# Optimization experiments

Hardware: AMD Instinct MI355X
Metric: run time of the kernel (lower is better)

The kernel has to match this reference:

```python
import jax, jax.numpy as jnp
import numpy as np

N, E, L, H, D_HID, D_IN, D_NEI, S_NEI, N_CLS = 30000, 480000, 2, 4, 128, 128, 64, 10, 2
HD = D_HID // H  # 32 per-head dim


def _mha(x, in_w, in_b, out_w, out_b, n_heads=4):
    # x: [N, S, D]; in_w: [D, 3D]; out_w: [D, D]
    n, s, d = x.shape
    hd = d // n_heads
    qkv = x @ in_w + in_b  # [N, S, 3D]
    q, k, v = jnp.split(qkv, 3, axis=-1)
    rs = lambda t: t.reshape(n, s, n_heads, hd).transpose(0, 2, 1, 3)  # [N,H,S,hd]
    q, k, v = rs(q), rs(k), rs(v)
    attn = jax.nn.softmax(jnp.einsum('nhqd,nhkd->nhqk', q, k) / np.sqrt(hd).astype(np.float32), axis=-1)
    o = jnp.einsum('nhqk,nhkd->nhqd', attn, v).transpose(0, 2, 1, 3).reshape(n, s, d)
    return o @ out_w + out_b


def _layer_norm(x, g, b, eps=1e-5):
    m = jnp.mean(x, axis=-1, keepdims=True)
    v = jnp.var(x, axis=-1, keepdims=True)
    return (x - m) * jax.lax.rsqrt(v + eps) * g + b


def _transformer_conv(src, dst, h, wq_i, bq_i, wk_i, bk_i, wv_i, bv_i):
    # per-head graph transformer conv: q from dst, k/v from src, edge softmax over dst
    q = (h @ wq_i + bq_i).reshape(N, H, HD)
    k = (h @ wk_i + bk_i).reshape(N, H, HD)
    v = (h @ wv_i + bv_i).reshape(N, H, HD)
    score = jnp.sum(q[dst] * k[src], axis=-1) / np.sqrt(HD).astype(np.float32)  # [E, H]
    smax = jax.ops.segment_max(score, dst, num_segments=N)  # [N, H]
    ex = jnp.exp(score - smax[dst])  # [E, H]
    denom = jax.ops.segment_sum(ex, dst, num_segments=N)  # [N, H]
    num = jax.ops.segment_sum(ex[:, :, None] * v[src], dst, num_segments=N)  # [N, H, HD]
    out = num / jnp.maximum(denom, 1e-9)[:, :, None]
    return out.reshape(N, D_HID)


def setup_inputs() -> dict:
    key = jax.random.key(0)
    ks = jax.random.split(key, 24)
    d = {}
    d['x'] = jax.random.normal(ks[0], (N, D_IN), jnp.float32)
    d['nei_features'] = jax.random.normal(ks[1], (N, S_NEI, D_NEI), jnp.float32)
    d['edge_index'] = jax.random.randint(ks[2], (L, 2, E), 0, N, jnp.int32)
    sc = 0.05
    d['w_in'] = jax.random.normal(ks[3], (D_IN, D_HID), jnp.float32) * sc
    d['b_in'] = jax.random.normal(ks[4], (D_HID,), jnp.float32) * sc
    d['mha_in_w'] = jax.random.normal(ks[5], (D_NEI, 3 * D_NEI), jnp.float32) * sc
    d['mha_in_b'] = jax.random.normal(ks[6], (3 * D_NEI,), jnp.float32) * sc
    d['mha_out_w'] = jax.random.normal(ks[7], (D_NEI, D_NEI), jnp.float32) * sc
    d['mha_out_b'] = jax.random.normal(ks[8], (D_NEI,), jnp.float32) * sc
    d['w_nei'] = jax.random.normal(ks[9], (D_NEI, D_HID), jnp.float32) * sc
    d['b_nei'] = jax.random.normal(ks[10], (D_HID,), jnp.float32) * sc
    d['wq'] = jax.random.normal(ks[11], (L, D_HID, D_HID), jnp.float32) * sc
    d['bq'] = jax.random.normal(ks[12], (L, D_HID), jnp.float32) * sc
    d['wk'] = jax.random.normal(ks[13], (L, D_HID, D_HID), jnp.float32) * sc
    d['bk'] = jax.random.normal(ks[14], (L, D_HID), jnp.float32) * sc
    d['wv'] = jax.random.normal(ks[15], (L, D_HID, D_HID), jnp.float32) * sc
    d['bv'] = jax.random.normal(ks[16], (L, D_HID), jnp.float32) * sc
    d['ln_g'] = jnp.ones((L, D_HID), jnp.float32)
    d['ln_b'] = jnp.zeros((L, D_HID), jnp.float32)
    d['w_out'] = jax.random.normal(ks[17], (D_HID, N_CLS), jnp.float32) * sc
    d['b_out'] = jnp.zeros((N_CLS,), jnp.float32)
    return d


def reference(x, nei_features, edge_index, w_in, b_in, mha_in_w, mha_in_b,
              mha_out_w, mha_out_b, w_nei, b_nei, wq, bq, wk, bk, wv, bv,
              ln_g, ln_b, w_out, b_out):
    h = x @ w_in + b_in  # input_proj
    # neighbor-feature self-attention branch (nn.MultiheadAttention, eval mode)
    nei = _mha(nei_features, mha_in_w, mha_in_b, mha_out_w, mha_out_b).mean(axis=1)
    h = h + (nei @ w_nei + b_nei)
    for i in range(L):
        src, dst = edge_index[i, 0], edge_index[i, 1]
        h = _transformer_conv(src, dst, h, wq[i], bq[i], wk[i], bk[i], wv[i], bv[i])
        h = jax.nn.relu(h)
        h = _layer_norm(h, ln_g[i], ln_b[i])
        # dropout is identity in eval mode
    return h @ w_out + b_out
```

## Files before the change

### kernel.cpp

```cpp
#include <hip/hip_runtime.h>
#include <hip/hip_bf16.h>

#define NN 30000
#define EE 480000

typedef __attribute__((ext_vector_type(8))) short short8;
typedef __attribute__((ext_vector_type(4))) short short4v;
typedef __attribute__((ext_vector_type(4))) float floatx4;
typedef unsigned short u16;

__device__ __forceinline__ u16 f2bf(float f) {
  union { float f; unsigned u; } v; v.f = f;
  unsigned u = v.u;
  u += 0x7FFFu + ((u >> 16) & 1u);
  return (u16)(u >> 16);
}
__device__ __forceinline__ float bf2f(u16 u) {
  union { unsigned u; float f; } v; v.u = ((unsigned)u) << 16;
  return v.f;
}
__device__ __forceinline__ float bflo(unsigned u) {
  union { unsigned x; float f; } v; v.x = u << 16; return v.f;
}
__device__ __forceinline__ float bfhi(unsigned u) {
  union { unsigned x; float f; } v; v.x = u & 0xFFFF0000u; return v.f;
}
__device__ __forceinline__ unsigned packbf(float a, float b) {
  return (unsigned)f2bf(a) | ((unsigned)f2bf(b) << 16);
}
__device__ __forceinline__ short8 pack8(float4 A, float4 B) {
  union { unsigned u[4]; short8 s; } r;
  r.u[0] = packbf(A.x, A.y);
  r.u[1] = packbf(A.z, A.w);
  r.u[2] = packbf(B.x, B.y);
  r.u[3] = packbf(B.z, B.w);
  return r.s;
}

template <int CTRL>
__device__ __forceinline__ float dppadd(float v) {
  int s = __builtin_amdgcn_update_dpp(0, __builtin_bit_cast(int, v), CTRL, 0xF, 0xF, true);
  return v + __builtin_bit_cast(float, s);
}
__device__ __forceinline__ float rowsum16(float v) {
  v = dppadd<0x121>(v); v = dppadd<0x122>(v); v = dppadd<0x124>(v); v = dppadd<0x128>(v);
  return v;
}
__device__ __forceinline__ float rowsum8(float v) {
  v = dppadd<0xB1>(v); v = dppadd<0x4E>(v); v = dppadd<0x141>(v);
  return v;
}

#define MFMA32 __builtin_amdgcn_mfma_f32_16x16x32_bf16

#if __has_builtin(__builtin_amdgcn_mfma_f32_16x16x16bf16_1k)
__device__ __forceinline__ floatx4 MFMA16(short4v a, short4v b, floatx4 c) {
  return __builtin_amdgcn_mfma_f32_16x16x16bf16_1k(a, b, c, 0, 0, 0);
}
#else
__device__ __forceinline__ floatx4 MFMA16(short4v a, short4v b, floatx4 c) {
  asm volatile("v_mfma_f32_16x16x16_bf16 %0, %1, %2, %0"
               : "+v"(c) : "v"(a), "v"(b));
  return c;
}
#endif

__global__ __launch_bounds__(128) void k_fuse(
    const float* __restrict__ out_w, const float* __restrict__ out_b,
    const float* __restrict__ w_nei, const float* __restrict__ b_nei,
    const float* __restrict__ b_in,
    float* __restrict__ fusedW, float* __restrict__ fusedB) {
  int i = blockIdx.x, j = threadIdx.x;
  if (i < 64) {
    float a = 0.f;
    for (int kk = 0; kk < 64; ++kk) a = fmaf(out_w[i * 64 + kk], w_nei[kk * 128 + j], a);
    fusedW[i * 128 + j] = a;
  } else {
    float a = b_in[j] + b_nei[j];
    for (int kk = 0; kk < 64; ++kk) a = fmaf(out_b[kk], w_nei[kk * 128 + j], a);
    fusedB[j] = a;
  }
}

__global__ __launch_bounds__(128) void k_prepB(
    const float* __restrict__ in_w, const float* __restrict__ fusedW,
    const float* __restrict__ fusedB, const float* __restrict__ in_b,
    float* __restrict__ G, float* __restrict__ fusedB2) {
  int bx = blockIdx.x, c = threadIdx.x;
  if (bx < 256) {
    int h = bx >> 6, d = bx & 63;
    float a = 0.f;
    for (int dd = 0; dd < 16; ++dd)
      a = fmaf(in_w[d * 192 + 128 + h * 16 + dd], fusedW[(h * 16 + dd) * 128 + c], a);
    G[bx * 128 + c] = a;
  } else {
    float a = fusedB[c];
    for (int d = 0; d < 64; ++d) a = fmaf(in_b[128 + d], fusedW[d * 128 + c], a);
    fusedB2[c] = a;
  }
}

__global__ __launch_bounds__(384) void k_prepP2(
    const float* __restrict__ w_in, const float* __restrict__ G,
    u16* __restrict__ wtP2) {
  int c = blockIdx.x, k = threadIdx.x;
  float v = (k < 128) ? w_in[(size_t)k * 128 + c] : G[(size_t)(k - 128) * 128 + c];
  wtP2[(size_t)c * 384 + k] = f2bf(v);
}

__global__ __launch_bounds__(128) void k_prepA(
    const float* __restrict__ wq, const float* __restrict__ wk,
    const float* __restrict__ wv, const float* __restrict__ in_w,
    u16* __restrict__ wt3, u16* __restrict__ wtQK) {
  int bx = blockIdx.x, t = threadIdx.x;
  if (bx < 768) {
    int l = bx / 384, rem = bx % 384, o = rem >> 7, c = rem & 127;
    const float* w = (o == 0 ? wq : (o == 1 ? wk : wv)) + (size_t)l * 16384;
    wt3[(size_t)bx * 128 + t] = f2bf(w[(size_t)t * 128 + c]);
  } else {
    int c = (bx - 768) * 2 + (t >> 6), kk = t & 63;
    float s = (c < 64) ? 0.25f : 1.f;
    wtQK[(size_t)c * 64 + kk] = f2bf(s * in_w[(size_t)kk * 192 + c]);
  }
}

__global__ __launch_bounds__(640) void k_mha7(
    const float* __restrict__ xn,
    const u16* __restrict__ wtQK,
    const float* __restrict__ in_b,
    u16* __restrict__ Yb) {
  __shared__ unsigned qks[112 * 66];
  __shared__ u16 xsT[64 * 160];
  int t = threadIdx.x, w = t >> 6, l = t & 63;
  int lr = l & 15, lq = l >> 4;
  const floatx4 zf = {0.f, 0.f, 0.f, 0.f};
  size_t r0 = (size_t)blockIdx.x * 100;

  {
    int d = t / 10, nd = t - d * 10;
#pragma unroll
    for (int j = 10; j < 16; ++j) xsT[d * 160 + nd * 16 + j] = 0;
  }

  if (w < 7) {
    int row = w * 16 + lr;
    size_t arow = r0 + row;
    if (arow > 299999) arow = 299999;
    const float* xp = xn + arow * 64 + lq * 8;
    float4 f0 = *(const float4*)xp;
    float4 f1 = *(const float4*)(xp + 4);
    float4 f2 = *(const float4*)(xp + 32);
    float4 f3 = *(const float4*)(xp + 36);
    short8 a0 = pack8(f0, f1), a1 = pack8(f2, f3);
    if (row < 100) {
      int node = row / 10, j = row - node * 10;
      int base = node * 16 + j;
      union { short8 s; u16 u[8]; } ua0, ua1;
      ua0.s = a0; ua1.s = a1;
#pragma unroll
      for (int i = 0; i < 8; ++i) {
        xsT[(lq * 8 + i) * 160 + base] = ua0.u[i];
        xsT[(32 + lq * 8 + i) * 160 + base] = ua1.u[i];
      }
    }
    floatx4 acc[8];
#pragma unroll
    for (int ct = 0; ct < 8; ++ct) acc[ct] = zf;
#pragma unroll
    for (int ct = 0; ct < 8; ++ct) {
      const short8* bp = (const short8*)(wtQK + (size_t)(ct * 16 + lr) * 64);
      acc[ct] = MFMA32(a0, bp[lq], acc[ct], 0, 0, 0);
      acc[ct] = MFMA32(a1, bp[4 + lq], acc[ct], 0, 0, 0);
    }
#pragma unroll
    for (int ct = 0; ct < 4; ++ct) {
      float bq_ = in_b[ct * 16 + lr] * 0.25f;
      float bk_ = in_b[64 + ct * 16 + lr];
#pragma unroll
      for (int r = 0; r < 4; ++r)
        qks[(w * 16 + lq * 4 + r) * 66 + ct * 16 + lr] =
            packbf(acc[ct][r] + bq_, acc[ct + 4][r] + bk_);
    }
  }
  __syncthreads();

  int seqc = lr < 10 ? lr : 9;
  {
    float af0 = 0.f, af1 = 0.f, af2 = 0.f, af3 = 0.f;
#pragma unroll
    for (int h = 0; h < 4; ++h) {
      const unsigned* rp = &qks[(w * 10 + seqc) * 66 + h * 16 + lq * 4];
      uint2 u0 = *(const uint2*)rp;
      uint2 u1 = *(const uint2*)(rp + 2);
      union { unsigned u[2]; short4v s; } qv, kv;
      qv.u[0] = (u0.x & 0xFFFFu) | (u0.y << 16);
      qv.u[1] = (u1.x & 0xFFFFu) | (u1.y << 16);
      kv.u[0] = (u0.x >> 16) | (u0.y & 0xFFFF0000u);
      kv.u[1] = (u1.x >> 16) | (u1.y & 0xFFFF0000u);
      floatx4 s4 = MFMA16(kv.s, qv.s, zf);
      int j0 = lq * 4;
      float e0 = (j0 + 0 < 10) ? __expf(s4[0]) : 0.f;
      float e1 = (j0 + 1 < 10) ? __expf(s4[1]) : 0.f;
      float e2 = (j0 + 2 < 10) ? __expf(s4[2]) : 0.f;
      float e3 = (j0 + 3 < 10) ? __expf(s4[3]) : 0.f;
      float den = e0 + e1 + e2 + e3;
      den += __shfl_xor(den, 16, 64);
      den += __shfl_xor(den, 32, 64);
      float rden = 0.1f / den;
      float v0 = (lr < 10) ? e0 * rden : 0.f;
      float v1 = (lr < 10) ? e1 * rden : 0.f;
      float v2 = (lr < 10) ? e2 * rden : 0.f;
      float v3 = (lr < 10) ? e3 * rden : 0.f;
      v0 = rowsum16(v0);
      v1 = rowsum16(v1);
      v2 = rowsum16(v2);
      v3 = rowsum16(v3);
      if (lr == h) { af0 = v0; af1 = v1; af2 = v2; af3 = v3; }
    }
    union { unsigned u[2]; short4v s; } afv;
    afv.u[0] = packbf(af0, af1);
    afv.u[1] = packbf(af2, af3);
    size_t node = (size_t)blockIdx.x * 10 + w;
#pragma unroll
    for (int ct = 0; ct < 4; ++ct) {
      short4v bx = *(const short4v*)&xsT[(ct * 16 + lr) * 160 + w * 16 + lq * 4];
      floatx4 y4 = MFMA16(afv.s, bx, zf);
      if (lq == 0) {
        size_t yb = node * 256;
#pragma unroll
        for (int r = 0; r < 4; ++r)
          Yb[yb + r * 64 + ct * 16 + lr] = f2bf(y4[r]);
      }
    }
  }
}

__global__ __launch_bounds__(256) void k_proj5(
    const float* __restrict__ x, const u16* __restrict__ Yb,
    const u16* __restrict__ wtP2, const float* __restrict__ fusedB2,
    u16* __restrict__ hb) {
  int t = threadIdx.x, w = t >> 6, l = t & 63, lr = l & 15, lq = l >> 4;
  int row0 = blockIdx.x * 64 + w * 16;
  int arow = row0 + lr; if (arow >= NN) arow = NN - 1;
  const float* xp = x + (size_t)arow * 128;
  const short8* yp = (const short8*)(Yb + (size_t)arow * 256);
  short8 afr[12];
#pragma unroll
  for (int kb = 0; kb < 4; ++kb) {
    float4 fa = *(const float4*)(xp + kb * 32 + lq * 8);
    float4 fb = *(const float4*)(xp + kb * 32 + lq * 8 + 4);
    afr[kb] = pack8(fa, fb);
  }
#pragma unroll
  for (int m = 0; m < 8; ++m) afr[4 + m] = yp[m * 4 + lq];
  floatx4 acc[8];
#pragma unroll
  for (int ct = 0; ct < 8; ++ct) acc[ct] = (floatx4){0.f, 0.f, 0.f, 0.f};
#pragma unroll
  for (int ct = 0; ct < 8; ++ct) {
    const short8* bp = (const short8*)(wtP2 + (size_t)(ct * 16 + lr) * 384);
#pragma unroll
    for (int kb = 0; kb < 12; ++kb)
      acc[ct] = MFMA32(afr[kb], bp[kb * 4 + lq], acc[ct], 0, 0, 0);
  }
#pragma unroll
  for (int ct = 0; ct < 8; ++ct) {
    int col = ct * 16 + lr;
    float bias = fusedB2[col];
#pragma unroll
    for (int r = 0; r < 4; ++r) {
      int row = row0 + lq * 4 + r;
      if (row < NN) hb[(size_t)row * 128 + col] = f2bf(acc[ct][r] + bias);
    }
  }
}

__global__ __launch_bounds__(256) void k_qkv4(
    const u16* __restrict__ hb, const u16* __restrict__ wt3l,
    const float* __restrict__ bqL, const float* __restrict__ bkL,
    const float* __restrict__ bvL,
    unsigned* __restrict__ q2, unsigned* __restrict__ k2, unsigned* __restrict__ v2) {
  int t = threadIdx.x, w = t >> 6, l = t & 63, lr = l & 15, lq = l >> 4;
  int row0 = blockIdx.x * 64 + w * 16;
  int arow = row0 + lr; if (arow >= NN) arow = NN - 1;
  const short8* ap = (const short8*)(hb + (size_t)arow * 128);
  short8 a0 = ap[lq], a1 = ap[4 + lq], a2 = ap[8 + lq], a3 = ap[12 + lq];
  const short8* wt8 = (const short8*)wt3l;
  floatx4 acc[24];
#pragma unroll
  for (int ct = 0; ct < 24; ++ct) acc[ct] = (floatx4){0.f, 0.f, 0.f, 0.f};
#pragma unroll
  for (int ct = 0; ct < 24; ++ct) {
    const short8* bp = wt8 + (size_t)((ct >> 3) * 128 + (ct & 7) * 16 + lr) * 16;
    acc[ct] = MFMA32(a0, bp[lq], acc[ct], 0, 0, 0);
    acc[ct] = MFMA32(a1, bp[4 + lq], acc[ct], 0, 0, 0);
    acc[ct] = MFMA32(a2, bp[8 + lq], acc[ct], 0, 0, 0);
    acc[ct] = MFMA32(a3, bp[12 + lq], acc[ct], 0, 0, 0);
  }
#pragma unroll
  for (int o = 0; o < 3; ++o) {
    unsigned* op = o == 0 ? q2 : (o == 1 ? k2 : v2);
    const float* bp2 = o == 0 ? bqL : (o == 1 ? bkL : bvL);
#pragma unroll
    for (int cc = 0; cc < 4; ++cc) {
      int col = cc * 16 + lr;
      float blo = bp2[col], bhi = bp2[64 + col];
      floatx4 alo = acc[o * 8 + cc], ahi = acc[o * 8 + cc + 4];
#pragma unroll
      for (int r = 0; r < 4; ++r) {
        int row = row0 + lq * 4 + r;
        if (row < NN)
          op[(size_t)row * 64 + col] = packbf(alo[r] + blo, ahi[r] + bhi);
      }
    }
  }
}

__global__ __launch_bounds__(256) void k_fill(const int* __restrict__ ei,
                                              int* __restrict__ cnt,
                                              int* __restrict__ esrc) {
  int gthr = blockIdx.x * 256 + threadIdx.x;
  if (gthr < 2 * EE) {
    int l = gthr >= EE;
    int e = gthr - l * EE;
    int s = ei[(size_t)(2 * l) * EE + e];
    int d = ei[(size_t)(2 * l + 1) * EE + e];
    int c = atomicAdd(&cnt[l * NN + d], 1);
    if (c < 64) esrc[((size_t)l * NN + d) * 64 + c] = s;
  }
}

__global__ __launch_bounds__(256) void k_sagg7(
    const unsigned* __restrict__ q2, const unsigned* __restrict__ k2,
    const unsigned* __restrict__ v2, const int* __restrict__ esrc,
    const int* __restrict__ cnt, const float* __restrict__ g,
    const float* __restrict__ bb, u16* __restrict__ hb,
    const float* __restrict__ wo, const float* __restrict__ bo,
    float* __restrict__ outp) {
  const float SC = 0.17677669529663687f;
  int t = threadIdx.x, w = t >> 6, l = t & 63;
  int e = l >> 4, dd = l & 15;
  int n = blockIdx.x * 4 + w;
  int deg = cnt[n]; if (deg > 64) deg = 64;
  const int* sp = esrc + (size_t)n * 64;
  uint4 qp = *(const uint4*)(q2 + (size_t)n * 64 + dd * 4);
  float ql0 = bflo(qp.x), ql1 = bflo(qp.y), ql2 = bflo(qp.z), ql3 = bflo(qp.w);
  float qh0 = bfhi(qp.x), qh1 = bfhi(qp.y), qh2 = bfhi(qp.z), qh3 = bfhi(qp.w);
  float dA0 = 0.f, dA1 = 0.f, dB0 = 0.f, dB1 = 0.f;
  float alA0 = 0.f, alA1 = 0.f, alA2 = 0.f, alA3 = 0.f;
  float ahA0 = 0.f, ahA1 = 0.f, ahA2 = 0.f, ahA3 = 0.f;
  float alB0 = 0.f, alB1 = 0.f, alB2 = 0.f, alB3 = 0.f;
  float ahB0 = 0.f, ahB1 = 0.f, ahB2 = 0.f, ahB3 = 0.f;
  uint4 kA = {0, 0, 0, 0}, vA = {0, 0, 0, 0};
  uint4 kB = {0, 0, 0, 0}, vB = {0, 0, 0, 0};
  bool mA = false, mB = false;
  if (deg > 0) {
    int iA = e < deg ? e : deg - 1;           mA = e < deg;
    int iB = 4 + e < deg ? 4 + e : deg - 1;   mB = 4 + e < deg;
    int sA = sp[iA], sB = sp[iB];
    kA = *(const uint4*)(k2 + (size_t)sA * 64 + dd * 4);
    vA = *(const uint4*)(v2 + (size_t)sA * 64 + dd * 4);
    kB = *(const uint4*)(k2 + (size_t)sB * 64 + dd * 4);
    vB = *(const uint4*)(v2 + (size_t)sB * 64 + dd * 4);
  }
  for (int base = 0; base < deg; base += 8) {
    uint4 kAn = {0, 0, 0, 0}, vAn = {0, 0, 0, 0};
    uint4 kBn = {0, 0, 0, 0}, vBn = {0, 0, 0, 0};
    bool mAn = false, mBn = false;
    int nb = base + 8;
    if (nb < deg) {
      int iA = nb + e < deg ? nb + e : deg - 1;         mAn = nb + e < deg;
      int iB = nb + 4 + e < deg ? nb + 4 + e : deg - 1; mBn = nb + 4 + e < deg;
      int sA = sp[iA], sB = sp[iB];
      kAn = *(const uint4*)(k2 + (size_t)sA * 64 + dd * 4);
      vAn = *(const uint4*)(v2 + (size_t)sA * 64 + dd * 4);
      kBn = *(const uint4*)(k2 + (size_t)sB * 64 + dd * 4);
      vBn = *(const uint4*)(v2 + (size_t)sB * 64 + dd * 4);
    }
    float rA0 = ql0 * bflo(kA.x) + ql1 * bflo(kA.y) + ql2 * bflo(kA.z) + ql3 * bflo(kA.w);
    float rA1 = qh0 * bfhi(kA.x) + qh1 * bfhi(kA.y) + qh2 * bfhi(kA.z) + qh3 * bfhi(kA.w);
    float rB0 = ql0 * bflo(kB.x) + ql1 * bflo(kB.y) + ql2 * bflo(kB.z) + ql3 * bflo(kB.w);
    float rB1 = qh0 * bfhi(kB.x) + qh1 * bfhi(kB.y) + qh2 * bfhi(kB.z) + qh3 * bfhi(kB.w);
    rA0 = rowsum8(rA0); rA1 = rowsum8(rA1);
    rB0 = rowsum8(rB0); rB1 = rowsum8(rB1);
    float pA0 = mA ? __expf(rA0 * SC) : 0.f;
    float pA1 = mA ? __expf(rA1 * SC) : 0.f;
    float pB0 = mB ? __expf(rB0 * SC) : 0.f;
    float pB1 = mB ? __expf(rB1 * SC) : 0.f;
    dA0 += pA0; dA1 += pA1; dB0 += pB0; dB1 += pB1;
    alA0 = fmaf(pA0, bflo(vA.x), alA0); alA1 = fmaf(pA0, bflo(vA.y), alA1);
    alA2 = fmaf(pA0, bflo(vA.z), alA2); alA3 = fmaf(pA0, bflo(vA.w), alA3);
    ahA0 = fmaf(pA1, bfhi(vA.x), ahA0); ahA1 = fmaf(pA1, bfhi(vA.y), ahA1);
    ahA2 = fmaf(pA1, bfhi(vA.z), ahA2); ahA3 = fmaf(pA1, bfhi(vA.w), ahA3);
    alB0 = fmaf(pB0, bflo(vB.x), alB0); alB1 = fmaf(pB0, bflo(vB.y), alB1);
    alB2 = fmaf(pB0, bflo(vB.z), alB2); alB3 = fmaf(pB0, bflo(vB.w), alB3);
    ahB0 = fmaf(pB1, bfhi(vB.x), ahB0); ahB1 = fmaf(pB1, bfhi(vB.y), ahB1);
    ahB2 = fmaf(pB1, bfhi(vB.z), ahB2); ahB3 = fmaf(pB1, bfhi(vB.w), ahB3);
    kA = kAn; vA = vAn; mA = mAn;
    kB = kBn; vB = vBn; mB = mBn;
  }
  float d0 = dA0 + dB0, d1 = dA1 + dB1;
  float al0 = alA0 + alB0, al1 = alA1 + alB1, al2 = alA2 + alB2, al3 = alA3 + alB3;
  float ah0 = ahA0 + ahB0, ah1 = ahA1 + ahB1, ah2 = ahA2 + ahB2, ah3 = ahA3 + ahB3;
  d0 += __shfl_xor(d0, 16, 64); d0 += __shfl_xor(d0, 32, 64);
  d1 += __shfl_xor(d1, 16, 64); d1 += __shfl_xor(d1, 32, 64);
  al0 += __shfl_xor(al0, 16, 64); al0 += __shfl_xor(al0, 32, 64);
  al1 += __shfl_xor(al1, 16, 64); al1 += __shfl_xor(al1, 32, 64);
  al2 += __shfl_xor(al2, 16, 64); al2 += __shfl_xor(al2, 32, 64);
  al3 += __shfl_xor(al3, 16, 64); al3 += __shfl_xor(al3, 32, 64);
  ah0 += __shfl_xor(ah0, 16, 64); ah0 += __shfl_xor(ah0, 32, 64);
  ah1 += __shfl_xor(ah1, 16, 64); ah1 += __shfl_xor(ah1, 32, 64);
  ah2 += __shfl_xor(ah2, 16, 64); ah2 += __shfl_xor(ah2, 32, 64);
  ah3 += __shfl_xor(ah3, 16, 64); ah3 += __shfl_xor(ah3, 32, 64);
  float rd0 = 1.f / fmaxf(d0, 1e-9f), rd1 = 1.f / fmaxf(d1, 1e-9f);
  float ol0 = fmaxf(al0 * rd0, 0.f), ol1 = fmaxf(al1 * rd0, 0.f);
  float ol2 = fmaxf(al2 * rd0, 0.f), ol3 = fmaxf(al3 * rd0, 0.f);
  float oh0 = fmaxf(ah0 * rd1, 0.f), oh1 = fmaxf(ah1 * rd1, 0.f);
  float oh2 = fmaxf(ah2 * rd1, 0.f), oh3 = fmaxf(ah3 * rd1, 0.f);
  float s1 = ol0 + ol1 + ol2 + ol3 + oh0 + oh1 + oh2 + oh3;
  float s2 = ol0 * ol0 + ol1 * ol1 + ol2 * ol2 + ol3 * ol3 +
             oh0 * oh0 + oh1 * oh1 + oh2 * oh2 + oh3 * oh3;
  s1 = rowsum16(s1);
  s2 = rowsum16(s2);
  float mean = s1 * (1.f / 128.f);
  float var = s2 * (1.f / 128.f) - mean * mean;
  float rs = rsqrtf(var + 1e-5f);
  if (e == 0) {
    floatx4 gl = *(const floatx4*)(g + dd * 4);
    floatx4 bl = *(const floatx4*)(bb + dd * 4);
    floatx4 gh = *(const floatx4*)(g + 64 + dd * 4);
    floatx4 bh = *(const floatx4*)(bb + 64 + dd * 4);
    float hl0 = (ol0 - mean) * rs * gl[0] + bl[0];
    float hl1 = (ol1 - mean) * rs * gl[1] + bl[1];
    float hl2 = (ol2 - mean) * rs * gl[2] + bl[2];
    float hl3 = (ol3 - mean) * rs * gl[3] + bl[3];
    float hh0 = (oh0 - mean) * rs * gh[0] + bh[0];
    float hh1 = (oh1 - mean) * rs * gh[1] + bh[1];
    float hh2 = (oh2 - mean) * rs * gh[2] + bh[2];
    float hh3 = (oh3 - mean) * rs * gh[3] + bh[3];
    if (outp == nullptr) {
      uint2 w0, w1;
      w0.x = packbf(hl0, hl1); w0.y = packbf(hl2, hl3);
      w1.x = packbf(hh0, hh1); w1.y = packbf(hh2, hh3);
      *(uint2*)(hb + (size_t)n * 128 + dd * 4) = w0;
      *(uint2*)(hb + (size_t)n * 128 + 64 + dd * 4) = w1;
    } else {
      const float2* wo2 = (const float2*)wo;
      float2 wa0 = wo2[dd * 4], wa1 = wo2[dd * 4 + 1];
      float2 wa2 = wo2[dd * 4 + 2], wa3 = wo2[dd * 4 + 3];
      float2 wb0 = wo2[64 + dd * 4], wb1 = wo2[64 + dd * 4 + 1];
      float2 wb2 = wo2[64 + dd * 4 + 2], wb3 = wo2[64 + dd * 4 + 3];
      float p0 = hl0 * wa0.x + hl1 * wa1.x + hl2 * wa2.x + hl3 * wa3.x +
                 hh0 * wb0.x + hh1 * wb1.x + hh2 * wb2.x + hh3 * wb3.x;
      float p1 = hl0 * wa0.y + hl1 * wa1.y + hl2 * wa2.y + hl3 * wa3.y +
                 hh0 * wb0.y + hh1 * wb1.y + hh2 * wb2.y + hh3 * wb3.y;
      p0 = rowsum16(p0);
      p1 = rowsum16(p1);
      if (dd == 0) {
        outp[n * 2] = p0 + bo[0];
        outp[n * 2 + 1] = p1 + bo[1];
      }
    }
  }
}

extern "C" void kernel_launch(void* const* d_in, const int* in_sizes, int n_in,
                              void* d_out, int out_size, void* d_ws, size_t ws_size,
                              hipStream_t stream) {
  const float* x = (const float*)d_in[0];
  const float* neif = (const float*)d_in[1];
  const int* ei = (const int*)d_in[2];
  const float* w_in = (const float*)d_in[3];
  const float* b_in = (const float*)d_in[4];
  const float* mha_in_w = (const float*)d_in[5];
  const float* mha_in_b = (const float*)d_in[6];
  const float* mha_out_w = (const float*)d_in[7];
  const float* mha_out_b = (const float*)d_in[8];
  const float* w_nei = (const float*)d_in[9];
  const float* b_nei = (const float*)d_in[10];
  const float* wq = (const float*)d_in[11];
  const float* bq = (const float*)d_in[12];
  const float* wk = (const float*)d_in[13];
  const float* bk = (const float*)d_in[14];
  const float* wv = (const float*)d_in[15];
  const float* bv = (const float*)d_in[16];
  const float* ln_g = (const float*)d_in[17];
  const float* ln_b = (const float*)d_in[18];
  const float* w_out = (const float*)d_in[19];
  const float* b_out = (const float*)d_in[20];
  float* out = (float*)d_out;

  char* wsb = (char*)d_ws;
  size_t off = 0;
  unsigned* q2 = (unsigned*)(wsb + off); off += (size_t)NN * 64 * 4;
  unsigned* k2 = (unsigned*)(wsb + off); off += (size_t)NN * 64 * 4;
  unsigned* v2 = (unsigned*)(wsb + off); off += (size_t)NN * 64 * 4;
  int* esrc = (int*)(wsb + off);         off += (size_t)2 * NN * 64 * 4;
  u16* Yb = (u16*)(wsb + off);           off += (size_t)NN * 256 * 2;
  u16* hb = (u16*)(wsb + off);           off += (size_t)NN * 128 * 2;
  u16* wt3 = (u16*)(wsb + off);          off += (size_t)768 * 128 * 2;
  u16* wtP2 = (u16*)(wsb + off);         off += (size_t)128 * 384 * 2;
  u16* wtQK = (u16*)(wsb + off);         off += (size_t)128 * 64 * 2;
  float* G = (float*)(wsb + off);        off += (size_t)256 * 128 * 4;
  float* fusedW = (float*)(wsb + off);   off += 64 * 128 * 4;
  float* fusedB = (float*)(wsb + off);   off += 128 * 4;
  float* fusedB2 = (float*)(wsb + off);  off += 128 * 4;
  int* cnt = (int*)(wsb + off);          off += (size_t)2 * NN * 4;

  k_fuse<<<65, 128, 0, stream>>>(mha_out_w, mha_out_b, w_nei, b_nei, b_in, fusedW, fusedB);
  k_prepB<<<257, 128, 0, stream>>>(mha_in_w, fusedW, fusedB, mha_in_b, G, fusedB2);
  k_prepP2<<<128, 384, 0, stream>>>(w_in, G, wtP2);
  k_prepA<<<832, 128, 0, stream>>>(wq, wk, wv, mha_in_w, wt3, wtQK);

  k_mha7<<<3000, 640, 0, stream>>>(neif, wtQK, mha_in_b, Yb);
  k_proj5<<<469, 256, 0, stream>>>(x, Yb, wtP2, fusedB2, hb);

  hipMemsetAsync(cnt, 0, 2 * NN * sizeof(int), stream);
  k_fill<<<3750, 256, 0, stream>>>(ei, cnt, esrc);

  for (int l = 0; l < 2; ++l) {
    k_qkv4<<<469, 256, 0, stream>>>(hb, wt3 + (size_t)l * 3 * 128 * 128,
                                    bq + l * 128, bk + l * 128, bv + l * 128,
                                    q2, k2, v2);
    k_sagg7<<<NN / 4, 256, 0, stream>>>(q2, k2, v2, esrc + (size_t)l * NN * 64,
                                        cnt + l * NN, ln_g + l * 128,
                                        ln_b + l * 128, hb,
                                        w_out, b_out, l == 0 ? nullptr : out);
  }
}
```

Before: 315.8 us.

## Fuse input projection with layer-0 QKV and simplify MHA output path

Merges the two weight-prep kernels into one launch. Replaces the MFMA-based attention-weighted sum in the MHA kernel with scalar FMAs over fp32 neighbor features, staging column sums in LDS. Fuses the input projection with the first layer's QKV GEMM so the hidden state stays in shared memory instead of round-tripping through global memory. The aim is fewer launches and less HBM traffic, at the cost of extra shared memory, more register pressure in the fused kernel, and re-reading neighbor features in fp32.

```diff
diff --git a/kernel.cpp b/kernel.cpp
--- a/kernel.cpp
+++ b/kernel.cpp
@@ -100,47 +100,43 @@
   }
 }
 
-__global__ __launch_bounds__(384) void k_prepP2(
+__global__ __launch_bounds__(128) void k_prep2(
     const float* __restrict__ w_in, const float* __restrict__ G,
-    u16* __restrict__ wtP2) {
-  int c = blockIdx.x, k = threadIdx.x;
-  float v = (k < 128) ? w_in[(size_t)k * 128 + c] : G[(size_t)(k - 128) * 128 + c];
-  wtP2[(size_t)c * 384 + k] = f2bf(v);
-}
-
-__global__ __launch_bounds__(128) void k_prepA(
     const float* __restrict__ wq, const float* __restrict__ wk,
     const float* __restrict__ wv, const float* __restrict__ in_w,
-    u16* __restrict__ wt3, u16* __restrict__ wtQK) {
+    u16* __restrict__ wtP2, u16* __restrict__ wt3, u16* __restrict__ wtQK) {
   int bx = blockIdx.x, t = threadIdx.x;
-  if (bx < 768) {
-    int l = bx / 384, rem = bx % 384, o = rem >> 7, c = rem & 127;
+  if (bx < 128) {
+    int c = bx;
+#pragma unroll
+    for (int part = 0; part < 3; ++part) {
+      int k = part * 128 + t;
+      float v = (k < 128) ? w_in[(size_t)k * 128 + c] : G[(size_t)(k - 128) * 128 + c];
+      wtP2[(size_t)c * 384 + k] = f2bf(v);
+    }
+  } else if (bx < 896) {
+    int b2 = bx - 128;
+    int l = b2 / 384, rem = b2 % 384, o = rem >> 7, c = rem & 127;
     const float* w = (o == 0 ? wq : (o == 1 ? wk : wv)) + (size_t)l * 16384;
-    wt3[(size_t)bx * 128 + t] = f2bf(w[(size_t)t * 128 + c]);
+    wt3[(size_t)b2 * 128 + t] = f2bf(w[(size_t)t * 128 + c]);
   } else {
-    int c = (bx - 768) * 2 + (t >> 6), kk = t & 63;
+    int c = (bx - 896) * 2 + (t >> 6), kk = t & 63;
     float s = (c < 64) ? 0.25f : 1.f;
     wtQK[(size_t)c * 64 + kk] = f2bf(s * in_w[(size_t)kk * 192 + c]);
   }
 }
 
-__global__ __launch_bounds__(640) void k_mha7(
+__global__ __launch_bounds__(640) void k_mha8(
     const float* __restrict__ xn,
     const u16* __restrict__ wtQK,
     const float* __restrict__ in_b,
     u16* __restrict__ Yb) {
   __shared__ unsigned qks[112 * 66];
-  __shared__ u16 xsT[64 * 160];
+  __shared__ float cs_lds[10][4][12];
   int t = threadIdx.x, w = t >> 6, l = t & 63;
   int lr = l & 15, lq = l >> 4;
   const floatx4 zf = {0.f, 0.f, 0.f, 0.f};
   size_t r0 = (size_t)blockIdx.x * 100;
-
-  {
-    int d = t / 10, nd = t - d * 10;
-#pragma unroll
-    for (int j = 10; j < 16; ++j) xsT[d * 160 + nd * 16 + j] = 0;
-  }
 
   if (w < 7) {
     int row = w * 16 + lr;
@@ -152,17 +148,6 @@
     float4 f2 = *(const float4*)(xp + 32);
     float4 f3 = *(const float4*)(xp + 36);
     short8 a0 = pack8(f0, f1), a1 = pack8(f2, f3);
-    if (row < 100) {
-      int node = row / 10, j = row - node * 10;
-      int base = node * 16 + j;
-      union { short8 s; u16 u[8]; } ua0, ua1;
-      ua0.s = a0; ua1.s = a1;
-#pragma unroll
-      for (int i = 0; i < 8; ++i) {
-        xsT[(lq * 8 + i) * 160 + base] = ua0.u[i];
-        xsT[(32 + lq * 8 + i) * 160 + base] = ua1.u[i];
-      }
-    }
     floatx4 acc[8];
 #pragma unroll
     for (int ct = 0; ct < 8; ++ct) acc[ct] = zf;
@@ -186,7 +171,6 @@
 
   int seqc = lr < 10 ? lr : 9;
   {
-    float af0 = 0.f, af1 = 0.f, af2 = 0.f, af3 = 0.f;
 #pragma unroll
     for (int h = 0; h < 4; ++h) {
       const unsigned* rp = &qks[(w * 10 + seqc) * 66 + h * 16 + lq * 4];
@@ -215,62 +199,108 @@
       v1 = rowsum16(v1);
       v2 = rowsum16(v2);
       v3 = rowsum16(v3);
-      if (lr == h) { af0 = v0; af1 = v1; af2 = v2; af3 = v3; }
-    }
-    union { unsigned u[2]; short4v s; } afv;
-    afv.u[0] = packbf(af0, af1);
-    afv.u[1] = packbf(af2, af3);
+      if (lr == 0) {
+        cs_lds[w][h][lq * 4 + 0] = v0;
+        cs_lds[w][h][lq * 4 + 1] = v1;
+        cs_lds[w][h][lq * 4 + 2] = v2;
+        cs_lds[w][h][lq * 4 + 3] = v3;
+      }
+    }
     size_t node = (size_t)blockIdx.x * 10 + w;
-#pragma unroll
-    for (int ct = 0; ct < 4; ++ct) {
-      short4v bx = *(const short4v*)&xsT[(ct * 16 + lr) * 160 + w * 16 + lq * 4];
-      floatx4 y4 = MFMA16(afv.s, bx, zf);
-      if (lq == 0) {
-        size_t yb = node * 256;
-#pragma unroll
-        for (int r = 0; r < 4; ++r)
-          Yb[yb + r * 64 + ct * 16 + lr] = f2bf(y4[r]);
-      }
-    }
-  }
-}
-
-__global__ __launch_bounds__(256) void k_proj5(
+    const float* xp2 = xn + node * 640 + l;
+    float y0 = 0.f, y1 = 0.f, y2 = 0.f, y3 = 0.f;
+#pragma unroll
+    for (int j = 0; j < 10; ++j) {
+      float xv = xp2[j * 64];
+      y0 = fmaf(cs_lds[w][0][j], xv, y0);
+      y1 = fmaf(cs_lds[w][1][j], xv, y1);
+      y2 = fmaf(cs_lds[w][2][j], xv, y2);
+      y3 = fmaf(cs_lds[w][3][j], xv, y3);
+    }
+    size_t yb = node * 256;
+    Yb[yb + l] = f2bf(y0);
+    Yb[yb + 64 + l] = f2bf(y1);
+    Yb[yb + 128 + l] = f2bf(y2);
+    Yb[yb + 192 + l] = f2bf(y3);
+  }
+}
+
+__global__ __launch_bounds__(256) void k_projqkv(
     const float* __restrict__ x, const u16* __restrict__ Yb,
     const u16* __restrict__ wtP2, const float* __restrict__ fusedB2,
-    u16* __restrict__ hb) {
+    const u16* __restrict__ wt3l,
+    const float* __restrict__ bqL, const float* __restrict__ bkL,
+    const float* __restrict__ bvL,
+    unsigned* __restrict__ q2, unsigned* __restrict__ k2, unsigned* __restrict__ v2) {
+  __shared__ u16 hs[64 * 128];
   int t = threadIdx.x, w = t >> 6, l = t & 63, lr = l & 15, lq = l >> 4;
   int row0 = blockIdx.x * 64 + w * 16;
   int arow = row0 + lr; if (arow >= NN) arow = NN - 1;
-  const float* xp = x + (size_t)arow * 128;
-  const short8* yp = (const short8*)(Yb + (size_t)arow * 256);
-  short8 afr[12];
-#pragma unroll
-  for (int kb = 0; kb < 4; ++kb) {
-    float4 fa = *(const float4*)(xp + kb * 32 + lq * 8);
-    float4 fb = *(const float4*)(xp + kb * 32 + lq * 8 + 4);
-    afr[kb] = pack8(fa, fb);
-  }
-#pragma unroll
-  for (int m = 0; m < 8; ++m) afr[4 + m] = yp[m * 4 + lq];
-  floatx4 acc[8];
-#pragma unroll
-  for (int ct = 0; ct < 8; ++ct) acc[ct] = (floatx4){0.f, 0.f, 0.f, 0.f};
-#pragma unroll
-  for (int ct = 0; ct < 8; ++ct) {
-    const short8* bp = (const short8*)(wtP2 + (size_t)(ct * 16 + lr) * 384);
-#pragma unroll
-    for (int kb = 0; kb < 12; ++kb)
-      acc[ct] = MFMA32(afr[kb], bp[kb * 4 + lq], acc[ct], 0, 0, 0);
-  }
-#pragma unroll
-  for (int ct = 0; ct < 8; ++ct) {
-    int col = ct * 16 + lr;
-    float bias = fusedB2[col];
-#pragma unroll
-    for (int r = 0; r < 4; ++r) {
-      int row = row0 + lq * 4 + r;
-      if (row < NN) hb[(size_t)row * 128 + col] = f2bf(acc[ct][r] + bias);
+  {
+    const float* xp = x + (size_t)arow * 128;
+    const short8* yp = (const short8*)(Yb + (size_t)arow * 256);
+    short8 afr[12];
+#pragma unroll
+    for (int kb = 0; kb < 4; ++kb) {
+      float4 fa = *(const float4*)(xp + kb * 32 + lq * 8);
+      float4 fb = *(const float4*)(xp + kb * 32 + lq * 8 + 4);
+      afr[kb] = pack8(fa, fb);
+    }
+#pragma unroll
+    for (int m = 0; m < 8; ++m) afr[4 + m] = yp[m * 4 + lq];
+    floatx4 acc[8];
+#pragma unroll
+    for (int ct = 0; ct < 8; ++ct) acc[ct] = (floatx4){0.f, 0.f, 0.f, 0.f};
+#pragma unroll
+    for (int ct = 0; ct < 8; ++ct) {
+      const short8* bp = (const short8*)(wtP2 + (size_t)(ct * 16 + lr) * 384);
+#pragma unroll
+      for (int kb = 0; kb < 12; ++kb)
+        acc[ct] = MFMA32(afr[kb], bp[kb * 4 + lq], acc[ct], 0, 0, 0);
+    }
+    int lrow = w * 16;
+#pragma unroll
+    for (int ct = 0; ct < 8; ++ct) {
+      int col = ct * 16 + lr;
+      float bias = fusedB2[col];
+#pragma unroll
+      for (int r = 0; r < 4; ++r)
+        hs[(lrow + lq * 4 + r) * 128 + col] = f2bf(acc[ct][r] + bias);
+    }
+  }
+  __syncthreads();
+  {
+    int lrow = w * 16 + lr;
+    const short8* ap = (const short8*)(hs + lrow * 128);
+    short8 a0 = ap[lq], a1 = ap[4 + lq], a2 = ap[8 + lq], a3 = ap[12 + lq];
+    const short8* wt8 = (const short8*)wt3l;
+    floatx4 acc[24];
+#pragma unroll
+    for (int ct = 0; ct < 24; ++ct) acc[ct] = (floatx4){0.f, 0.f, 0.f, 0.f};
+#pragma unroll
+    for (int ct = 0; ct < 24; ++ct) {
+      const short8* bp = wt8 + (size_t)((ct >> 3) * 128 + (ct & 7) * 16 + lr) * 16;
+      acc[ct] = MFMA32(a0, bp[lq], acc[ct], 0, 0, 0);
+      acc[ct] = MFMA32(a1, bp[4 + lq], acc[ct], 0, 0, 0);
+      acc[ct] = MFMA32(a2, bp[8 + lq], acc[ct], 0, 0, 0);
+      acc[ct] = MFMA32(a3, bp[12 + lq], acc[ct], 0, 0, 0);
+    }
+#pragma unroll
+    for (int o = 0; o < 3; ++o) {
+      unsigned* op = o == 0 ? q2 : (o == 1 ? k2 : v2);
+      const float* bp2 = o == 0 ? bqL : (o == 1 ? bkL : bvL);
+#pragma unroll
+      for (int cc = 0; cc < 4; ++cc) {
+        int col = cc * 16 + lr;
+        float blo = bp2[col], bhi = bp2[64 + col];
+        floatx4 alo = acc[o * 8 + cc], ahi = acc[o * 8 + cc + 4];
+#pragma unroll
+        for (int r = 0; r < 4; ++r) {
+          int row = row0 + lq * 4 + r;
+          if (row < NN)
+            op[(size_t)row * 64 + col] = packbf(alo[r] + blo, ahi[r] + bhi);
+        }
+      }
     }
   }
 }
@@ -509,22 +539,20 @@
 
   k_fuse<<<65, 128, 0, stream>>>(mha_out_w, mha_out_b, w_nei, b_nei, b_in, fusedW, fusedB);
   k_prepB<<<257, 128, 0, stream>>>(mha_in_w, fusedW, fusedB, mha_in_b, G, fusedB2);
-  k_prepP2<<<128, 384, 0, stream>>>(w_in, G, wtP2);
-  k_prepA<<<832, 128, 0, stream>>>(wq, wk, wv, mha_in_w, wt3, wtQK);
-
-  k_mha7<<<3000, 640, 0, stream>>>(neif, wtQK, mha_in_b, Yb);
-  k_proj5<<<469, 256, 0, stream>>>(x, Yb, wtP2, fusedB2, hb);
+  k_prep2<<<960, 128, 0, stream>>>(w_in, G, wq, wk, wv, mha_in_w, wtP2, wt3, wtQK);
+
+  k_mha8<<<3000, 640, 0, stream>>>(neif, wtQK, mha_in_b, Yb);
 
   hipMemsetAsync(cnt, 0, 2 * NN * sizeof(int), stream);
   k_fill<<<3750, 256, 0, stream>>>(ei, cnt, esrc);
 
-  for (int l = 0; l < 2; ++l) {
-    k_qkv4<<<469, 256, 0, stream>>>(hb, wt3 + (size_t)l * 3 * 128 * 128,
-                                    bq + l * 128, bk + l * 128, bv + l * 128,
-                                    q2, k2, v2);
-    k_sagg7<<<NN / 4, 256, 0, stream>>>(q2, k2, v2, esrc + (size_t)l * NN * 64,
-                                        cnt + l * NN, ln_g + l * 128,
-                                        ln_b + l * 128, hb,
-                                        w_out, b_out, l == 0 ? nullptr : out);
-  }
-}
+  k_projqkv<<<469, 256, 0, stream>>>(x, Yb, wtP2, fusedB2, wt3,
+                                     bq, bk, bv, q2, k2, v2);
+  k_sagg7<<<NN / 4, 256, 0, stream>>>(q2, k2, v2, esrc, cnt,
+                                      ln_g, ln_b, hb, w_out, b_out, nullptr);
+  k_qkv4<<<469, 256, 0, stream>>>(hb, wt3 + (size_t)3 * 128 * 128,
+                                  bq + 128, bk + 128, bv + 128, q2, k2, v2);
+  k_sagg7<<<NN / 4, 256, 0, stream>>>(q2, k2, v2, esrc + (size_t)NN * 64,
+                                      cnt + NN, ln_g + 128, ln_b + 128, hb,
+                                      w_out, b_out, out);
+}
```

Result: faster. 300.0 us (-5.0%).
